# Performance work log

Measured on AMD Instinct MI355X. Metric: run time of the kernel, lower is better.

## Reference

```python
import jax, jax.numpy as jnp
import numpy as np

D_MODEL, EMB_DIM, ORDER, SEQ_LEN, BATCH = 768, 33, 64, 8192, 2


def setup_inputs() -> dict:
    key = jax.random.key(0)
    ks = jax.random.split(key, 9)
    x = jax.random.normal(ks[0], (BATCH, D_MODEL, SEQ_LEN), dtype=jnp.float32)

    # PositionalEmbedding: t in [0,1], complex exponential bands
    bands = (EMB_DIM - 1) // 2
    t = jnp.linspace(0.0, 1.0, SEQ_LEN, dtype=jnp.float32)[None, :, None]          # (1, L, 1)
    t_rescaled = jnp.linspace(0.0, SEQ_LEN - 1, SEQ_LEN, dtype=jnp.float32)[None, :, None]
    w_ang = 2.0 * jnp.pi * t_rescaled / SEQ_LEN                                     # (1, L, 1)
    f = jnp.linspace(1e-4, bands - 1, bands, dtype=jnp.float32)[None, None]         # (1, 1, bands)
    zc = jnp.exp(-1j * f.astype(jnp.complex64) * w_ang.astype(jnp.complex64))
    z = jnp.concatenate([t, zc.real, zc.imag], axis=-1)                             # (1, L, emb_dim)

    # Sin activation frequency (shared single instance across all MLP layers), w=1
    freq = jnp.ones((1, ORDER), dtype=jnp.float32)

    def lin(k, fan_out, fan_in):
        s = 1.0 / np.sqrt(fan_in)
        return jax.random.normal(k, (fan_out, fan_in), dtype=jnp.float32) * s

    W1 = lin(ks[1], ORDER, EMB_DIM)
    b1 = jax.random.normal(ks[2], (ORDER,), dtype=jnp.float32) * 0.02
    W2 = lin(ks[3], ORDER, ORDER)
    b2 = jax.random.normal(ks[4], (ORDER,), dtype=jnp.float32) * 0.02
    W3 = lin(ks[5], ORDER, ORDER)
    b3 = jax.random.normal(ks[6], (ORDER,), dtype=jnp.float32) * 0.02
    Wout = lin(ks[7], D_MODEL, ORDER)  # no bias

    # ExponentialModulation deltas (deterministic buffer)
    target, fast_pct, slow_pct = 0.01, 0.3, 1.5
    max_decay = np.log(target) / fast_pct
    min_decay = np.log(target) / slow_pct
    deltas = jnp.linspace(min_decay, max_decay, D_MODEL, dtype=jnp.float32)[None, None]  # (1,1,d)

    bias_D = jax.random.normal(ks[8], (D_MODEL,), dtype=jnp.float32)

    return {"x": x, "L": SEQ_LEN, "z": z, "t": t, "freq": freq,
            "W1": W1, "b1": b1, "W2": W2, "b2": b2, "W3": W3, "b3": b3,
            "Wout": Wout, "deltas": deltas, "bias_D": bias_D}


def reference(x, L, z, t, freq, W1, b1, W2, b2, W3, b3, Wout, deltas, bias_D):
    zL, tL = z[:, :L], t[:, :L]                      # (1, L, emb_dim), (1, L, 1)
    # Implicit filter MLP with shared Sin activation
    h = jnp.sin(freq * (jnp.einsum('ble,oe->blo', zL, W1) + b1))
    h = jnp.sin(freq * (jnp.einsum('blo,po->blp', h, W2) + b2))
    h = jnp.sin(freq * (jnp.einsum('blo,po->blp', h, W3) + b3))
    h = jnp.einsum('blo,do->bld', h, Wout)           # (1, L, d_model)
    # Exponential modulation
    h = h * jnp.exp(-tL * jnp.abs(deltas))
    k = h[0].T                                       # (d_model, L)
    # FFT-based long convolution (fftconv_ref with gelu=False).
    # torch: k_f = rfft(k, n)/n ; y = irfft(u_f*k_f, n, norm='forward') == standard irfft(u_f*rfft(k,n), n)
    fft_size = 2 * L
    k_f = jnp.fft.rfft(k, n=fft_size)                # (d_model, n//2+1) complex
    u_f = jnp.fft.rfft(x, n=fft_size)                # (B, d_model, n//2+1)
    y = jnp.fft.irfft(u_f * k_f, n=fft_size)[..., :L]
    out = y + x * bias_D[:, None]
    return out.astype(x.dtype)
```

## Files before the change

### kernel.cpp

```cpp
#include <hip/hip_runtime.h>
#include <hip/hip_fp16.h>
#include <math.h>

#define D_MODEL 768
#define EMB 33
#define ORDER 64
#define SEQ 8192
#define BATCH 2
#define M 8192

#define PI_F 3.14159265358979323846f

#define IDX(a) ((a) + ((a) >> 4) + ((a) >> 7))
#define LDS_SZ 8768

__device__ __forceinline__ int rev13(int x) { return (int)(__brev((unsigned)x) >> 19); }

__device__ __constant__ float C8[8] = {
    1.f, 0.9238795325f, 0.7071067812f, 0.3826834324f,
    0.f, -0.3826834324f, -0.7071067812f, -0.9238795325f };
__device__ __constant__ float S8n[8] = {
    0.f, -0.3826834324f, -0.7071067812f, -0.9238795325f,
    -1.f, -0.9238795325f, -0.7071067812f, -0.3826834324f };
__device__ __constant__ float S8p[8] = {
    0.f, 0.3826834324f, 0.7071067812f, 0.9238795325f,
    1.f, 0.9238795325f, 0.7071067812f, 0.3826834324f };

__global__ __launch_bounds__(256) void mlp_kernel(
    const float* __restrict__ z, const float* __restrict__ freq,
    const float* __restrict__ W1, const float* __restrict__ b1,
    const float* __restrict__ W2, const float* __restrict__ b2,
    const float* __restrict__ W3, const float* __restrict__ b3,
    float* __restrict__ h3out)
{
    __shared__ float sz[64 * 33];
    __shared__ float sW1[64 * 33];
    __shared__ float sW2[64 * 64];
    __shared__ float sW3[64 * 64];
    __shared__ float hA[64 * 65];
    __shared__ float hB[64 * 65];
    __shared__ float sb1[64], sb2[64], sb3[64], sfr[64];
    int t = threadIdx.x;
    int l0 = blockIdx.x * 64;
    for (int i = t; i < 2112; i += 256) { sz[i] = z[(size_t)l0 * 33 + i]; sW1[i] = W1[i]; }
    for (int i = t; i < 4096; i += 256) { sW2[i] = W2[i]; sW3[i] = W3[i]; }
    if (t < 64) { sb1[t] = b1[t]; sb2[t] = b2[t]; sb3[t] = b3[t]; sfr[t] = freq[t]; }
    __syncthreads();

    int l = t & 63, grp = t >> 6;
    float acc[16];
#pragma unroll
    for (int i = 0; i < 16; ++i) {
        int o = grp * 16 + i;
        float a = sb1[o];
        for (int e = 0; e < 33; ++e) a = fmaf(sz[l * 33 + e], sW1[o * 33 + e], a);
        acc[i] = __sinf(sfr[o] * a);
    }
#pragma unroll
    for (int i = 0; i < 16; ++i) hA[l * 65 + grp * 16 + i] = acc[i];
    __syncthreads();
#pragma unroll
    for (int i = 0; i < 16; ++i) {
        int o = grp * 16 + i;
        float a = sb2[o];
        for (int q = 0; q < 64; ++q) a = fmaf(hA[l * 65 + q], sW2[o * 64 + q], a);
        acc[i] = __sinf(sfr[o] * a);
    }
#pragma unroll
    for (int i = 0; i < 16; ++i) hB[l * 65 + grp * 16 + i] = acc[i];
    __syncthreads();
#pragma unroll
    for (int i = 0; i < 16; ++i) {
        int o = grp * 16 + i;
        float a = sb3[o];
        for (int q = 0; q < 64; ++q) a = fmaf(hB[l * 65 + q], sW3[o * 64 + q], a);
        acc[i] = __sinf(sfr[o] * a);
    }
#pragma unroll
    for (int i = 0; i < 16; ++i) hA[l * 65 + grp * 16 + i] = acc[i];
    __syncthreads();
    for (int i = t; i < 4096; i += 256) {
        int ll = i >> 6, o = i & 63;
        h3out[(size_t)l0 * 64 + i] = hA[ll * 65 + o];
    }
}

__global__ __launch_bounds__(256) void filt_kernel(
    const float* __restrict__ h3, const float* __restrict__ Wout,
    const float* __restrict__ tvec, const float* __restrict__ deltas,
    float* __restrict__ kout)
{
    __shared__ float hs[64][65];
    __shared__ float wsm[64][65];
    int t = threadIdx.x;
    int l0 = blockIdx.x * 64, d0 = blockIdx.y * 64;
    for (int m = t; m < 4096; m += 256) {
        int r = m >> 6, c = m & 63;
        hs[r][c] = h3[(size_t)(l0 + r) * 64 + c];
        wsm[r][c] = Wout[(size_t)(d0 + r) * 64 + c];
    }
    __syncthreads();
    int tx = t & 63, ty = t >> 6;
    float acc[16];
#pragma unroll
    for (int i = 0; i < 16; i++) acc[i] = 0.f;
#pragma unroll
    for (int kk = 0; kk < 64; kk++) {
        float hv = hs[tx][kk];
#pragma unroll
        for (int i = 0; i < 16; i++) acc[i] = fmaf(hv, wsm[ty * 16 + i][kk], acc[i]);
    }
    float tl = tvec[l0 + tx];
#pragma unroll
    for (int i = 0; i < 16; i++) {
        int d = d0 + ty * 16 + i;
        float kv = acc[i] * __expf(-tl * fabsf(deltas[d]));
        kout[(size_t)d * SEQ + l0 + tx] = kv;
    }
}

template<int H>
__device__ __forceinline__ void fwd8(float* Ar, float* Ai, int t)
{
    constexpr int H4 = H / 4;
    int j0 = t & (H4 - 1);
    float c1, s1;
    __sincosf((-PI_F / (float)H) * (float)j0, &s1, &c1);
#pragma unroll
    for (int gg = 0; gg < 2; ++gg) {
        int g = t + (gg << 9);
        int j = g & (H4 - 1);
        int i = ((g & ~(H4 - 1)) << 3) | j;
        float c1g = c1, s1g = s1;
        if (H4 > 512 && gg == 1) {
            const float cR = 0.9238795325f, sR = -0.3826834324f;
            c1g = c1 * cR - s1 * sR;
            s1g = s1 * cR + c1 * sR;
        }
        float c2 = c1g * c1g - s1g * s1g, s2 = 2.f * c1g * s1g;
        float c3 = c2 * c2 - s2 * s2,     s3 = 2.f * c2 * s2;
        float xr[8], xi[8];
        int ad[8];
#pragma unroll
        for (int m = 0; m < 8; ++m) { ad[m] = IDX(i + m * H4); xr[m] = Ar[ad[m]]; xi[m] = Ai[ad[m]]; }
        const float r = 0.70710678118f;
        float twc[4], tws[4];
        twc[0] = c1g;             tws[0] = s1g;
        twc[1] = r * (c1g + s1g); tws[1] = r * (s1g - c1g);
        twc[2] = s1g;             tws[2] = -c1g;
        twc[3] = r * (s1g - c1g); tws[3] = -r * (c1g + s1g);
#pragma unroll
        for (int m = 0; m < 4; ++m) {
            float ur = xr[m] + xr[m + 4], ui = xi[m] + xi[m + 4];
            float dr = xr[m] - xr[m + 4], di = xi[m] - xi[m + 4];
            xr[m] = ur; xi[m] = ui;
            xr[m + 4] = dr * twc[m] - di * tws[m];
            xi[m + 4] = dr * tws[m] + di * twc[m];
        }
#pragma unroll
        for (int base = 0; base < 8; base += 4)
#pragma unroll
            for (int mm = 0; mm < 2; ++mm) {
                int a = base + mm, b = a + 2;
                float ur = xr[a] + xr[b], ui = xi[a] + xi[b];
                float dr = xr[a] - xr[b], di = xi[a] - xi[b];
                xr[a] = ur; xi[a] = ui;
                if (mm == 0) { xr[b] = dr * c2 - di * s2; xi[b] = dr * s2 + di * c2; }
                else         { xr[b] = dr * s2 + di * c2; xi[b] = di * s2 - dr * c2; }
            }
#pragma unroll
        for (int m = 0; m < 8; m += 2) {
            float ur = xr[m] + xr[m + 1], ui = xi[m] + xi[m + 1];
            float dr = xr[m] - xr[m + 1], di = xi[m] - xi[m + 1];
            xr[m] = ur; xi[m] = ui;
            xr[m + 1] = dr * c3 - di * s3; xi[m + 1] = dr * s3 + di * c3;
        }
#pragma unroll
        for (int m = 0; m < 8; ++m) { Ar[ad[m]] = xr[m]; Ai[ad[m]] = xi[m]; }
    }
}

template<int H>
__device__ __forceinline__ void inv8(float* Ar, float* Ai, int t)
{
    int j0 = t & (H - 1);
    float ct, st;
    __sincosf((PI_F / (float)(4 * H)) * (float)j0, &st, &ct);
#pragma unroll
    for (int gg = 0; gg < 2; ++gg) {
        int g = t + (gg << 9);
        int j = g & (H - 1);
        int i = ((g & ~(H - 1)) << 3) | j;
        float c = ct, s = st;
        if (H > 512 && gg == 1) {
            const float cR = 0.9238795325f, sR = 0.3826834324f;
            c = ct * cR - st * sR;
            s = st * cR + ct * sR;
        }
        float c2 = c * c - s * s, s2 = 2.f * c * s;
        float c4 = c2 * c2 - s2 * s2, s4 = 2.f * c2 * s2;
        float xr[8], xi[8]; int ad[8];
#pragma unroll
        for (int m = 0; m < 8; ++m) { ad[m] = IDX(i + m * H); xr[m] = Ar[ad[m]]; xi[m] = Ai[ad[m]]; }
#pragma unroll
        for (int m = 0; m < 8; m += 2) {
            float tr = xr[m + 1] * c4 - xi[m + 1] * s4;
            float ti = xr[m + 1] * s4 + xi[m + 1] * c4;
            xr[m + 1] = xr[m] - tr; xi[m + 1] = xi[m] - ti;
            xr[m]     = xr[m] + tr; xi[m]     = xi[m] + ti;
        }
#pragma unroll
        for (int base = 0; base < 8; base += 4)
#pragma unroll
            for (int mm = 0; mm < 2; ++mm) {
                int a = base + mm, b = a + 2;
                float tr, ti;
                if (mm == 0) { tr = xr[b] * c2 - xi[b] * s2; ti = xr[b] * s2 + xi[b] * c2; }
                else         { tr = -(xr[b] * s2 + xi[b] * c2); ti = xr[b] * c2 - xi[b] * s2; }
                xr[b] = xr[a] - tr; xi[b] = xi[a] - ti;
                xr[a] = xr[a] + tr; xi[a] = xi[a] + ti;
            }
        const float r = 0.70710678118f;
        float t3c[4], t3s[4];
        t3c[0] = c;           t3s[0] = s;
        t3c[1] = r * (c - s); t3s[1] = r * (c + s);
        t3c[2] = -s;          t3s[2] = c;
        t3c[3] = -r * (c + s); t3s[3] = r * (c - s);
#pragma unroll
        for (int m = 0; m < 4; ++m) {
            float tr = xr[m + 4] * t3c[m] - xi[m + 4] * t3s[m];
            float ti = xr[m + 4] * t3s[m] + xi[m + 4] * t3c[m];
            xr[m + 4] = xr[m] - tr; xi[m + 4] = xi[m] - ti;
            xr[m]     = xr[m] + tr; xi[m]     = xi[m] + ti;
        }
#pragma unroll
        for (int m = 0; m < 8; ++m) { Ar[ad[m]] = xr[m]; Ai[ad[m]] = xi[m]; }
    }
}

__device__ __forceinline__ void fft_fwd(float* Ar, float* Ai, int t)
{
    fwd8<4096>(Ar, Ai, t); __syncthreads();
    fwd8<512>(Ar, Ai, t);  __syncthreads();
    fwd8<64>(Ar, Ai, t);   __syncthreads();
    {
        int pb = IDX(16 * t);
        float fr[16], fi[16];
#pragma unroll
        for (int e = 0; e < 16; ++e) { fr[e] = Ar[pb + e]; fi[e] = Ai[pb + e]; }
#pragma unroll
        for (int k = 0; k < 8; ++k) {
            float cs = C8[k], sn = S8n[k];
            float arr = fr[k], aii = fi[k], brr = fr[k + 8], bii = fi[k + 8];
            fr[k] = arr + brr; fi[k] = aii + bii;
            float dr = arr - brr, di = aii - bii;
            fr[k + 8] = dr * cs - di * sn; fi[k + 8] = dr * sn + di * cs;
        }
#pragma unroll
        for (int b0 = 0; b0 < 16; b0 += 8)
#pragma unroll
            for (int k = 0; k < 4; ++k) {
                float cs = C8[2 * k], sn = S8n[2 * k];
                int i0 = b0 + k, i1 = i0 + 4;
                float arr = fr[i0], aii = fi[i0], brr = fr[i1], bii = fi[i1];
                fr[i0] = arr + brr; fi[i0] = aii + bii;
                float dr = arr - brr, di = aii - bii;
                fr[i1] = dr * cs - di * sn; fi[i1] = dr * sn + di * cs;
            }
#pragma unroll
        for (int b0 = 0; b0 < 16; b0 += 4)
#pragma unroll
            for (int k = 0; k < 2; ++k) {
                float cs = C8[4 * k], sn = S8n[4 * k];
                int i0 = b0 + k, i1 = i0 + 2;
                float arr = fr[i0], aii = fi[i0], brr = fr[i1], bii = fi[i1];
                fr[i0] = arr + brr; fi[i0] = aii + bii;
                float dr = arr - brr, di = aii - bii;
                fr[i1] = dr * cs - di * sn; fi[i1] = dr * sn + di * cs;
            }
#pragma unroll
        for (int b0 = 0; b0 < 16; b0 += 2) {
            float arr = fr[b0], aii = fi[b0], brr = fr[b0 + 1], bii = fi[b0 + 1];
            fr[b0] = arr + brr; fi[b0] = aii + bii;
            fr[b0 + 1] = arr - brr; fi[b0 + 1] = aii - bii;
        }
#pragma unroll
        for (int e = 0; e < 16; ++e) { Ar[pb + e] = fr[e]; Ai[pb + e] = fi[e]; }
        __syncthreads();
    }
}

__device__ __forceinline__ void fft_inv(float* Ar, float* Ai, int t)
{
    {
        int pb = IDX(16 * t);
        float fr[16], fi[16];
#pragma unroll
        for (int e = 0; e < 16; ++e) { fr[e] = Ar[pb + e]; fi[e] = Ai[pb + e]; }
#pragma unroll
        for (int b0 = 0; b0 < 16; b0 += 2) {
            float arr = fr[b0], aii = fi[b0], brr = fr[b0 + 1], bii = fi[b0 + 1];
            fr[b0] = arr + brr; fi[b0] = aii + bii;
            fr[b0 + 1] = arr - brr; fi[b0 + 1] = aii - bii;
        }
#pragma unroll
        for (int b0 = 0; b0 < 16; b0 += 4)
#pragma unroll
            for (int k = 0; k < 2; ++k) {
                float cs = C8[4 * k], sn = S8p[4 * k];
                int i0 = b0 + k, i1 = i0 + 2;
                float arr = fr[i0], aii = fi[i0], brr = fr[i1], bii = fi[i1];
                float tr = brr * cs - bii * sn, ti = brr * sn + bii * cs;
                fr[i0] = arr + tr; fi[i0] = aii + ti;
                fr[i1] = arr - tr; fi[i1] = aii - ti;
            }
#pragma unroll
        for (int b0 = 0; b0 < 16; b0 += 8)
#pragma unroll
            for (int k = 0; k < 4; ++k) {
                float cs = C8[2 * k], sn = S8p[2 * k];
                int i0 = b0 + k, i1 = i0 + 4;
                float arr = fr[i0], aii = fi[i0], brr = fr[i1], bii = fi[i1];
                float tr = brr * cs - bii * sn, ti = brr * sn + bii * cs;
                fr[i0] = arr + tr; fi[i0] = aii + ti;
                fr[i1] = arr - tr; fi[i1] = aii - ti;
            }
#pragma unroll
        for (int k = 0; k < 8; ++k) {
            float cs = C8[k], sn = S8p[k];
            float arr = fr[k], aii = fi[k], brr = fr[k + 8], bii = fi[k + 8];
            float tr = brr * cs - bii * sn, ti = brr * sn + bii * cs;
            fr[k] = arr + tr; fi[k] = aii + ti;
            fr[k + 8] = arr - tr; fi[k + 8] = aii - ti;
        }
#pragma unroll
        for (int e = 0; e < 16; ++e) { Ar[pb + e] = fr[e]; Ai[pb + e] = fi[e]; }
        __syncthreads();
    }
    inv8<16>(Ar, Ai, t);   __syncthreads();
    inv8<128>(Ar, Ai, t);  __syncthreads();
    inv8<1024>(Ar, Ai, t); __syncthreads();
}

__global__ __launch_bounds__(512, 4) void kf_kernel(float* outk)
{
    __shared__ float Are[LDS_SZ], Aim[LDS_SZ];
    int t = threadIdx.x, d = blockIdx.x;
    const float* kp = outk + (size_t)d * SEQ;
    for (int n = t; n < 4096; n += 512) {
        float2 v = ((const float2*)kp)[n];
        Are[IDX(n)] = v.x; Aim[IDX(n)] = v.y;
    }
    for (int n = 4096 + t; n < M; n += 512) { Are[IDX(n)] = 0.f; Aim[IDX(n)] = 0.f; }
    __syncthreads();
    fft_fwd(Are, Aim, t);

    __half2* P0 = (__half2*)(outk + (size_t)d * SEQ);
    __half2* P1 = (__half2*)(outk + (size_t)(D_MODEL + d) * SEQ);
    float cs, sn;
    __sincosf(-PI_F * (float)t * (1.0f / 8192.0f), &sn, &cs);
    const float cRo = 0.9807852804f, sRo = -0.1950903220f;
    for (int j = t; j <= 4096; j += 512) {
        int jm = (M - j) & (M - 1);
        int p0 = rev13(j), p1 = rev13(jm);
        float z1r = Are[IDX(p0)], z1i = Aim[IDX(p0)];
        float z2r = Are[IDX(p1)], z2i = Aim[IDX(p1)];
        float Ar_ = 0.5f * (z1r + z2r), Ai_ = 0.5f * (z1i - z2i);
        float Br_ = 0.5f * (z1i + z2i), Bi_ = 0.5f * (z2r - z1r);
        float wbr = cs * Br_ - sn * Bi_, wbi = cs * Bi_ + sn * Br_;
        float K1r = Ar_ + wbr, K1i = Ai_ + wbi;
        float K2r = Ar_ - wbr, K2i = -(Ai_ - wbi);
        if (j == 0) {
            __half2 v = __floats2half2_rn(K1r, K2r);
            P0[0] = v; P1[0] = v;
        } else {
            __half2 v1 = __floats2half2_rn(K1r, K1i);
            P0[j] = v1; P1[j] = v1;
            if (j != 4096) {
                __half2 v2 = __floats2half2_rn(K2r, K2i);
                P0[M - j] = v2; P1[M - j] = v2;
            }
        }
        float cn = cs * cRo - sn * sRo; sn = sn * cRo + cs * sRo; cs = cn;
    }
}

__global__ __launch_bounds__(512, 4) void conv_kernel(
    const float* __restrict__ x, const float* __restrict__ bias,
    float* outk)
{
    __shared__ float Are[LDS_SZ], Aim[LDS_SZ];
    int t = threadIdx.x, d = blockIdx.x, b = blockIdx.y;
    const float* xp = x + ((size_t)(b * D_MODEL + d)) * SEQ;

    float2 xv[8];
#pragma unroll
    for (int idx = 0; idx < 8; ++idx) {
        int n = t + (idx << 9);
        xv[idx] = ((const float2*)xp)[n];
        Are[IDX(n)] = xv[idx].x; Aim[IDX(n)] = xv[idx].y;
    }
    for (int n = 4096 + t; n < M; n += 512) { Are[IDX(n)] = 0.f; Aim[IDX(n)] = 0.f; }
    __syncthreads();
    fft_fwd(Are, Aim, t);

    const __half2* P = (const __half2*)(outk + (size_t)(b * D_MODEL + d) * SEQ);
    float cs, sn;
    __sincosf(-PI_F * (float)t * (1.0f / 8192.0f), &sn, &cs);
    const float cRo = 0.9807852804f, sRo = -0.1950903220f;
    for (int j = t; j <= 4096; j += 512) {
        int jm = (M - j) & (M - 1);
        int p0 = rev13(j), p1 = rev13(jm);
        int q0 = IDX(p0), q1 = IDX(p1);
        float z1r = Are[q0], z1i = Aim[q0];
        float z2r = Are[q1], z2i = Aim[q1];
        float Ar_ = 0.5f * (z1r + z2r), Ai_ = 0.5f * (z1i - z2i);
        float Br_ = 0.5f * (z1i + z2i), Bi_ = 0.5f * (z2r - z1r);
        float wbr = cs * Br_ - sn * Bi_, wbi = cs * Bi_ + sn * Br_;
        float U1r = Ar_ + wbr, U1i = Ai_ + wbi;
        float U2r = Ar_ - wbr, U2i = -(Ai_ - wbi);
        float K1r, K1i, K2r, K2i;
        if (j == 0) {
            __half2 v = P[0];
            K1r = __low2float(v);  K1i = 0.f;
            K2r = __high2float(v); K2i = 0.f;
        } else {
            __half2 v1 = P[j];
            __half2 v2 = P[M - j];
            K1r = __low2float(v1); K1i = __high2float(v1);
            K2r = __low2float(v2); K2i = __high2float(v2);
        }
        float P1r = U1r * K1r - U1i * K1i, P1i = U1r * K1i + U1i * K1r;
        float P2r = U2r * K2r - U2i * K2i, P2i = U2r * K2i + U2i * K2r;
        float Er = 0.5f * (P1r + P2r), Ei = 0.5f * (P1i - P2i);
        float Or = 0.5f * (P1r - P2r), Oi = 0.5f * (P1i + P2i);
        float G = cs * Oi - sn * Or;
        float H = cs * Or + sn * Oi;
        Are[q0] = Er - G; Aim[q0] = Ei + H;
        if (j != 0) { Are[q1] = Er + G; Aim[q1] = -Ei + H; }
        float cn = cs * cRo - sn * sRo; sn = sn * cRo + cs * sRo; cs = cn;
    }
    __syncthreads();
    fft_inv(Are, Aim, t);

    const float invM = 1.0f / 8192.0f;
    float bd = bias[d];
    float* op = outk + ((size_t)(b * D_MODEL + d)) * SEQ;
#pragma unroll
    for (int idx = 0; idx < 8; ++idx) {
        int n = t + (idx << 9);
        float2 ov;
        ov.x = fmaf(Are[IDX(n)], invM, xv[idx].x * bd);
        ov.y = fmaf(Aim[IDX(n)], invM, xv[idx].y * bd);
        ((float2*)op)[n] = ov;
    }
}

extern "C" void kernel_launch(void* const* d_in, const int* in_sizes, int n_in,
                              void* d_out, int out_size, void* d_ws, size_t ws_size,
                              hipStream_t stream)
{
    (void)in_sizes; (void)n_in; (void)out_size; (void)d_ws; (void)ws_size;
    const float* x      = (const float*)d_in[0];
    const float* z      = (const float*)d_in[2];
    const float* tvec   = (const float*)d_in[3];
    const float* freq   = (const float*)d_in[4];
    const float* W1     = (const float*)d_in[5];
    const float* b1     = (const float*)d_in[6];
    const float* W2     = (const float*)d_in[7];
    const float* b2     = (const float*)d_in[8];
    const float* W3     = (const float*)d_in[9];
    const float* b3     = (const float*)d_in[10];
    const float* Wout   = (const float*)d_in[11];
    const float* deltas = (const float*)d_in[12];
    const float* bias   = (const float*)d_in[13];
    float* out = (float*)d_out;

    float* h3 = out + ((size_t)(2 * D_MODEL - 64) * SEQ);
    float* k  = out;

    hipLaunchKernelGGL(mlp_kernel, dim3(SEQ / 64), dim3(256), 0, stream,
                       z, freq, W1, b1, W2, b2, W3, b3, h3);
    hipLaunchKernelGGL(filt_kernel, dim3(SEQ / 64, D_MODEL / 64), dim3(256), 0, stream,
                       h3, Wout, tvec, deltas, k);
    hipLaunchKernelGGL(kf_kernel, dim3(D_MODEL), dim3(512), 0, stream, out);
    hipLaunchKernelGGL(conv_kernel, dim3(D_MODEL, BATCH), dim3(512), 0, stream,
                       x, bias, out);
}
```

Baseline: 262.3 us.

## Register-tile MLP and filter GEMMs with transposed intermediate and float4 LDS access

The MLP layers become 4x4 register-blocked outer products over transposed LDS tiles, with weights staged one layer at a time to cut shared memory. The hidden output is written transposed (order x seq) so the filter kernel can read it coalesced. The filter GEMM now uses 128-wide sequence tiles with 4x8 register blocking and float4 stores. The goal is fewer LDS loads per FMA and better global coalescing in the filter-generation stage, which is probably a small part of total time next to the FFT kernels.

```diff
diff --git a/kernel.cpp b/kernel.cpp
--- a/kernel.cpp
+++ b/kernel.cpp
@@ -31,91 +31,161 @@
     const float* __restrict__ W1, const float* __restrict__ b1,
     const float* __restrict__ W2, const float* __restrict__ b2,
     const float* __restrict__ W3, const float* __restrict__ b3,
-    float* __restrict__ h3out)
-{
-    __shared__ float sz[64 * 33];
-    __shared__ float sW1[64 * 33];
-    __shared__ float sW2[64 * 64];
-    __shared__ float sW3[64 * 64];
-    __shared__ float hA[64 * 65];
-    __shared__ float hB[64 * 65];
-    __shared__ float sb1[64], sb2[64], sb3[64], sfr[64];
+    float* __restrict__ h3T)
+{
+    __shared__ float zt[33 * 72];
+    __shared__ float h1[64 * 72];
+    __shared__ float h2[64 * 72];
+    __shared__ float Wb[64 * 68];
+    __shared__ float sfr[64], sb[64];
     int t = threadIdx.x;
     int l0 = blockIdx.x * 64;
-    for (int i = t; i < 2112; i += 256) { sz[i] = z[(size_t)l0 * 33 + i]; sW1[i] = W1[i]; }
-    for (int i = t; i < 4096; i += 256) { sW2[i] = W2[i]; sW3[i] = W3[i]; }
-    if (t < 64) { sb1[t] = b1[t]; sb2[t] = b2[t]; sb3[t] = b3[t]; sfr[t] = freq[t]; }
-    __syncthreads();
-
-    int l = t & 63, grp = t >> 6;
-    float acc[16];
-#pragma unroll
-    for (int i = 0; i < 16; ++i) {
-        int o = grp * 16 + i;
-        float a = sb1[o];
-        for (int e = 0; e < 33; ++e) a = fmaf(sz[l * 33 + e], sW1[o * 33 + e], a);
-        acc[i] = __sinf(sfr[o] * a);
-    }
-#pragma unroll
-    for (int i = 0; i < 16; ++i) hA[l * 65 + grp * 16 + i] = acc[i];
-    __syncthreads();
-#pragma unroll
-    for (int i = 0; i < 16; ++i) {
-        int o = grp * 16 + i;
-        float a = sb2[o];
-        for (int q = 0; q < 64; ++q) a = fmaf(hA[l * 65 + q], sW2[o * 64 + q], a);
-        acc[i] = __sinf(sfr[o] * a);
-    }
-#pragma unroll
-    for (int i = 0; i < 16; ++i) hB[l * 65 + grp * 16 + i] = acc[i];
-    __syncthreads();
-#pragma unroll
-    for (int i = 0; i < 16; ++i) {
-        int o = grp * 16 + i;
-        float a = sb3[o];
-        for (int q = 0; q < 64; ++q) a = fmaf(hB[l * 65 + q], sW3[o * 64 + q], a);
-        acc[i] = __sinf(sfr[o] * a);
-    }
-#pragma unroll
-    for (int i = 0; i < 16; ++i) hA[l * 65 + grp * 16 + i] = acc[i];
-    __syncthreads();
+
+    for (int i = t; i < 64 * 33; i += 256) {
+        int l = i / 33, e = i - l * 33;
+        zt[e * 72 + l] = z[(size_t)(l0 + l) * 33 + e];
+    }
+    for (int i = t; i < 64 * 33; i += 256) {
+        int o = i / 33, e = i - o * 33;
+        Wb[e * 68 + o] = W1[i];
+    }
+    if (t < 64) { sfr[t] = freq[t]; sb[t] = b1[t]; }
+    __syncthreads();
+
+    int lx = t & 15, oy = t >> 4;
+    float fr4[4], bi4[4], acc[4][4];
+#pragma unroll
+    for (int i = 0; i < 4; ++i) { fr4[i] = sfr[4 * oy + i]; bi4[i] = sb[4 * oy + i]; }
+#pragma unroll
+    for (int c = 0; c < 4; ++c)
+#pragma unroll
+        for (int i = 0; i < 4; ++i) acc[c][i] = bi4[i];
+    for (int e = 0; e < 33; ++e) {
+        float4 hv = *(const float4*)&zt[e * 72 + 4 * lx];
+        float4 wv = *(const float4*)&Wb[e * 68 + 4 * oy];
+        float h[4] = {hv.x, hv.y, hv.z, hv.w}, w[4] = {wv.x, wv.y, wv.z, wv.w};
+#pragma unroll
+        for (int c = 0; c < 4; ++c)
+#pragma unroll
+            for (int i = 0; i < 4; ++i) acc[c][i] = fmaf(h[c], w[i], acc[c][i]);
+    }
+#pragma unroll
+    for (int i = 0; i < 4; ++i) {
+        float4 v = make_float4(__sinf(fr4[i] * acc[0][i]), __sinf(fr4[i] * acc[1][i]),
+                               __sinf(fr4[i] * acc[2][i]), __sinf(fr4[i] * acc[3][i]));
+        *(float4*)&h1[(4 * oy + i) * 72 + 4 * lx] = v;
+    }
+    __syncthreads();
+
     for (int i = t; i < 4096; i += 256) {
-        int ll = i >> 6, o = i & 63;
-        h3out[(size_t)l0 * 64 + i] = hA[ll * 65 + o];
+        int o = i >> 6, q = i & 63;
+        Wb[q * 68 + o] = W2[i];
+    }
+    if (t < 64) sb[t] = b2[t];
+    __syncthreads();
+#pragma unroll
+    for (int i = 0; i < 4; ++i) bi4[i] = sb[4 * oy + i];
+#pragma unroll
+    for (int c = 0; c < 4; ++c)
+#pragma unroll
+        for (int i = 0; i < 4; ++i) acc[c][i] = bi4[i];
+    for (int q = 0; q < 64; ++q) {
+        float4 hv = *(const float4*)&h1[q * 72 + 4 * lx];
+        float4 wv = *(const float4*)&Wb[q * 68 + 4 * oy];
+        float h[4] = {hv.x, hv.y, hv.z, hv.w}, w[4] = {wv.x, wv.y, wv.z, wv.w};
+#pragma unroll
+        for (int c = 0; c < 4; ++c)
+#pragma unroll
+            for (int i = 0; i < 4; ++i) acc[c][i] = fmaf(h[c], w[i], acc[c][i]);
+    }
+#pragma unroll
+    for (int i = 0; i < 4; ++i) {
+        float4 v = make_float4(__sinf(fr4[i] * acc[0][i]), __sinf(fr4[i] * acc[1][i]),
+                               __sinf(fr4[i] * acc[2][i]), __sinf(fr4[i] * acc[3][i]));
+        *(float4*)&h2[(4 * oy + i) * 72 + 4 * lx] = v;
+    }
+    __syncthreads();
+
+    for (int i = t; i < 4096; i += 256) {
+        int o = i >> 6, q = i & 63;
+        Wb[q * 68 + o] = W3[i];
+    }
+    if (t < 64) sb[t] = b3[t];
+    __syncthreads();
+#pragma unroll
+    for (int i = 0; i < 4; ++i) bi4[i] = sb[4 * oy + i];
+#pragma unroll
+    for (int c = 0; c < 4; ++c)
+#pragma unroll
+        for (int i = 0; i < 4; ++i) acc[c][i] = bi4[i];
+    for (int q = 0; q < 64; ++q) {
+        float4 hv = *(const float4*)&h2[q * 72 + 4 * lx];
+        float4 wv = *(const float4*)&Wb[q * 68 + 4 * oy];
+        float h[4] = {hv.x, hv.y, hv.z, hv.w}, w[4] = {wv.x, wv.y, wv.z, wv.w};
+#pragma unroll
+        for (int c = 0; c < 4; ++c)
+#pragma unroll
+            for (int i = 0; i < 4; ++i) acc[c][i] = fmaf(h[c], w[i], acc[c][i]);
+    }
+#pragma unroll
+    for (int i = 0; i < 4; ++i) {
+        float4 v = make_float4(__sinf(fr4[i] * acc[0][i]), __sinf(fr4[i] * acc[1][i]),
+                               __sinf(fr4[i] * acc[2][i]), __sinf(fr4[i] * acc[3][i]));
+        *(float4*)&h3T[(size_t)(4 * oy + i) * SEQ + l0 + 4 * lx] = v;
     }
 }
 
 __global__ __launch_bounds__(256) void filt_kernel(
-    const float* __restrict__ h3, const float* __restrict__ Wout,
+    const float* __restrict__ h3T, const float* __restrict__ Wout,
     const float* __restrict__ tvec, const float* __restrict__ deltas,
     float* __restrict__ kout)
 {
-    __shared__ float hs[64][65];
-    __shared__ float wsm[64][65];
+    __shared__ float ht[64 * 132];
+    __shared__ float wt[64 * 68];
     int t = threadIdx.x;
-    int l0 = blockIdx.x * 64, d0 = blockIdx.y * 64;
-    for (int m = t; m < 4096; m += 256) {
-        int r = m >> 6, c = m & 63;
-        hs[r][c] = h3[(size_t)(l0 + r) * 64 + c];
-        wsm[r][c] = Wout[(size_t)(d0 + r) * 64 + c];
-    }
-    __syncthreads();
-    int tx = t & 63, ty = t >> 6;
-    float acc[16];
-#pragma unroll
-    for (int i = 0; i < 16; i++) acc[i] = 0.f;
-#pragma unroll
-    for (int kk = 0; kk < 64; kk++) {
-        float hv = hs[tx][kk];
-#pragma unroll
-        for (int i = 0; i < 16; i++) acc[i] = fmaf(hv, wsm[ty * 16 + i][kk], acc[i]);
-    }
-    float tl = tvec[l0 + tx];
-#pragma unroll
-    for (int i = 0; i < 16; i++) {
-        int d = d0 + ty * 16 + i;
-        float kv = acc[i] * __expf(-tl * fabsf(deltas[d]));
-        kout[(size_t)d * SEQ + l0 + tx] = kv;
+    int l0 = blockIdx.x * 128, d0 = blockIdx.y * 64;
+
+    for (int i = t; i < 64 * 128; i += 256) {
+        int o = i >> 7, l = i & 127;
+        ht[o * 132 + l] = h3T[(size_t)o * SEQ + l0 + l];
+    }
+    for (int i = t; i < 4096; i += 256) {
+        int dd = i >> 6, kk = i & 63;
+        wt[kk * 68 + dd] = Wout[(size_t)(d0 + dd) * 64 + kk];
+    }
+    __syncthreads();
+
+    int lx = t & 31, dy = t >> 5;
+    float acc[4][8];
+#pragma unroll
+    for (int c = 0; c < 4; ++c)
+#pragma unroll
+        for (int i = 0; i < 8; ++i) acc[c][i] = 0.f;
+    for (int kk = 0; kk < 64; ++kk) {
+        float4 hv = *(const float4*)&ht[kk * 132 + 4 * lx];
+        float4 w0 = *(const float4*)&wt[kk * 68 + 8 * dy];
+        float4 w1 = *(const float4*)&wt[kk * 68 + 8 * dy + 4];
+        float h[4] = {hv.x, hv.y, hv.z, hv.w};
+        float w[8] = {w0.x, w0.y, w0.z, w0.w, w1.x, w1.y, w1.z, w1.w};
+#pragma unroll
+        for (int c = 0; c < 4; ++c)
+#pragma unroll
+            for (int i = 0; i < 8; ++i) acc[c][i] = fmaf(h[c], w[i], acc[c][i]);
+    }
+
+    float4 tl4 = *(const float4*)&tvec[l0 + 4 * lx];
+    float tl[4] = {tl4.x, tl4.y, tl4.z, tl4.w};
+    float del[8];
+#pragma unroll
+    for (int i = 0; i < 8; ++i) del[i] = fabsf(deltas[d0 + 8 * dy + i]);
+#pragma unroll
+    for (int i = 0; i < 8; ++i) {
+        int d = d0 + 8 * dy + i;
+        float4 v = make_float4(acc[0][i] * __expf(-tl[0] * del[i]),
+                               acc[1][i] * __expf(-tl[1] * del[i]),
+                               acc[2][i] * __expf(-tl[2] * del[i]),
+                               acc[3][i] * __expf(-tl[3] * del[i]));
+        *(float4*)&kout[(size_t)d * SEQ + l0 + 4 * lx] = v;
     }
 }
 
@@ -476,13 +546,13 @@
     const float* bias   = (const float*)d_in[13];
     float* out = (float*)d_out;
 
-    float* h3 = out + ((size_t)(2 * D_MODEL - 64) * SEQ);
-    float* k  = out;
+    float* h3T = out + ((size_t)(2 * D_MODEL - 64) * SEQ);
+    float* k   = out;
 
     hipLaunchKernelGGL(mlp_kernel, dim3(SEQ / 64), dim3(256), 0, stream,
-                       z, freq, W1, b1, W2, b2, W3, b3, h3);
-    hipLaunchKernelGGL(filt_kernel, dim3(SEQ / 64, D_MODEL / 64), dim3(256), 0, stream,
-                       h3, Wout, tvec, deltas, k);
+                       z, freq, W1, b1, W2, b2, W3, b3, h3T);
+    hipLaunchKernelGGL(filt_kernel, dim3(SEQ / 128, D_MODEL / 64), dim3(256), 0, stream,
+                       h3T, Wout, tvec, deltas, k);
     hipLaunchKernelGGL(kf_kernel, dim3(D_MODEL), dim3(512), 0, stream, out);
     hipLaunchKernelGGL(conv_kernel, dim3(D_MODEL, BATCH), dim3(512), 0, stream,
                        x, bias, out);
```

After: 245.2 us. -6.5%, faster.
